# Kernel optimization log

Measured on AMD Instinct MI355X. Metric: run time of the kernel, lower is better.

The kernel has to match this reference:

```python
import jax, jax.numpy as jnp
import numpy as np

I_DIM, K_DIM, V_DIM, O_DIM = 64, 64, 32, 64
P, NH, NK = 7, 2, 4
B, H, W = 8, 256, 256


def get_unfold_params_v2(width, kernel_size, num_kernels):
    # exact replica of the torch helper's search
    if width <= kernel_size:
        return width, 1, 1, 1
    if width <= kernel_size + num_kernels:
        return kernel_size, 1, 1, width - kernel_size + 1

    def _sd(nk):
        d = 1
        while True:
            k = (kernel_size - 1) * d + 1
            if (width - k) % (nk - 1) == 0:
                return (width - k) // (nk - 1), d
            d += 1
            if d >= kernel_size:
                return None, d

    while True:
        s, d = _sd(num_kernels)
        if s and s < (kernel_size - 1) * d + 1:
            return kernel_size, s, d, num_kernels
        num_kernels += 1


def conv1x1(x, Wt, b):
    # x: [B,C,H,W], Wt: [O,C]
    return jnp.einsum('oc,bchw->bohw', Wt, x) + b[None, :, None, None]


def to_patches(x, nh, idx, p):
    # x: [B,C,H,W] -> [B, nh, nph*npw, C//nh, p*p] (unfold + rearrange)
    Bs, C, _, _ = x.shape
    hd = C // nh
    npw = idx.shape[0]
    pt = x[:, :, idx][:, :, :, :, idx]          # [B,C,nph,ph,npw,pw]
    pt = pt.reshape(Bs, nh, hd, npw, p, npw, p)
    pt = pt.transpose(0, 1, 3, 5, 2, 4, 6)       # B,nh,nph,npw,hd,ph,pw
    return pt.reshape(Bs, nh, npw * npw, hd, p * p)


def from_patches(o, nh, idx, p, Hh, Ww):
    # o: [B,nh,S,hd,p*p] -> fold (overlap scatter-add) -> [B, nh*hd, H, W]
    Bs, _, _, hd, _ = o.shape
    npw = idx.shape[0]
    o = o.reshape(Bs, nh, npw, npw, hd, p, p)
    o = o.transpose(0, 1, 4, 2, 5, 3, 6)         # B,nh,hd,nph,ph,npw,pw
    o = o.reshape(Bs, nh * hd, npw, p, npw, p)
    out = jnp.zeros((Bs, nh * hd, Hh, Ww), o.dtype)
    return out.at[:, :, idx[:, :, None, None], idx[None, None, :, :]].add(o)


def setup_inputs() -> dict:
    key = jax.random.key(0)
    ks = jax.random.split(key, 8)
    s = 0.05
    return {
        'x1': jax.random.normal(ks[0], (B, I_DIM, H, W), jnp.float32),
        'x2': jax.random.normal(ks[1], (B, I_DIM, H, W), jnp.float32),
        'Wk': jax.random.normal(ks[2], (2 * K_DIM, I_DIM), jnp.float32) * s,
        'bk': jax.random.normal(ks[3], (2 * K_DIM,), jnp.float32) * s,
        'Wv': jax.random.normal(ks[4], (2 * V_DIM, I_DIM), jnp.float32) * s,
        'bv': jax.random.normal(ks[5], (2 * V_DIM,), jnp.float32) * s,
        'Wp': jax.random.normal(ks[6], (O_DIM, 2 * V_DIM), jnp.float32) * s,
        'bp': jax.random.normal(ks[7], (O_DIM,), jnp.float32) * s,
    }


def reference(x1, x2, Wk, bk, Wv, bv, Wp, bp):
    _, _, Hh, Ww = x1.shape
    p, stride, dilation, nkrn = get_unfold_params_v2(Ww, P, NK)
    idx = np.arange(nkrn)[:, None] * stride + np.arange(p)[None, :] * dilation  # [npw,p]

    # grouped 1x1 convs (groups=2): split weights into per-stream halves
    k1 = conv1x1(x1, Wk[:K_DIM], bk[:K_DIM])
    k2 = conv1x1(x2, Wk[K_DIM:], bk[K_DIM:])
    v1 = conv1x1(x1, Wv[:V_DIM], bv[:V_DIM])
    v2 = conv1x1(x2, Wv[V_DIM:], bv[V_DIM:])

    k1p = to_patches(k1, NH, idx, p)  # [B,nh,S,hd_k,pp]
    k2p = to_patches(k2, NH, idx, p)
    v1p = to_patches(v1, NH, idx, p)  # [B,nh,S,hd_v,pp]
    v2p = to_patches(v2, NH, idx, p)

    scale = k1p.shape[-2] ** (-0.5)
    kk = jnp.einsum('bnsdx,bnsdy->bnsxy', k1p * scale, k2p)  # [B,nh,S,pp,pp]
    a1 = jax.nn.softmax(kk, axis=-2)
    o1 = jnp.einsum('bnsxy,bnsdx->bnsdy', a1, v1p)
    a2 = jax.nn.softmax(kk, axis=-1)
    o2 = jnp.einsum('bnsxy,bnsdy->bnsdx', a2, v2p)

    o1 = from_patches(o1, NH, idx, p, Hh, Ww)  # [B,V_DIM,H,W]
    o2 = from_patches(o2, NH, idx, p, Hh, Ww)
    o = jnp.concatenate([o1, o2], axis=1)      # [B,2*V_DIM,H,W]
    return conv1x1(o, Wp, bp)                  # [B,O_DIM,H,W]
```

## Files before the change

### kernel.cpp

```cpp
#include <hip/hip_runtime.h>

#define BB 8
#define HH 256
#define CIN 64
#define NPW 12
#define SPP 144
#define PP 49
#define PDIM 7
#define STRIDE 21
#define DIL 4
#define NS 84

typedef __attribute__((ext_vector_type(8))) short bf16x8;
typedef __attribute__((ext_vector_type(4))) float f32x4;

#define MFMA(a, b, c) __builtin_amdgcn_mfma_f32_16x16x32_bf16((a), (b), (c), 0, 0, 0)

static __device__ __forceinline__ unsigned short f2bf(float f) {
  union { float f; unsigned u; } v; v.f = f;
  unsigned r = (v.u + 0x7fffu + ((v.u >> 16) & 1u)) >> 16;
  return (unsigned short)r;
}
static __device__ __forceinline__ float bf2f(unsigned short h) {
  union { unsigned u; float f; } v; v.u = ((unsigned)h) << 16;
  return v.f;
}
static __device__ __forceinline__ unsigned pk2(float a, float b) {
  return (unsigned)f2bf(a) | ((unsigned)f2bf(b) << 16);
}

__global__ __launch_bounds__(256, 3) void k1_fused(
    const float* __restrict__ x1, const float* __restrict__ x2,
    const float* __restrict__ Wk, const float* __restrict__ bk,
    const float* __restrict__ Wv, const float* __restrict__ bv,
    const float* __restrict__ Wp, float* __restrict__ P)
{
  __shared__ __align__(16) short uA[9216];
  __shared__ __align__(16) short uB[8704];
  __shared__ __align__(16) short sV[4096];
  __shared__ float sStat[4][2][64];

  const int tid = threadIdx.x;
  const int lane = tid & 63;
  const int wid = tid >> 6;
  const int l16 = lane & 15;
  const int l4 = lane >> 4;
  const int blk = blockIdx.x;
  const int b  = blk / SPP;
  const int sp = blk % SPP;
  const int pi = sp / NPW, pj = sp % NPW;
  const int h0 = pi * STRIDE, w0 = pj * STRIDE;

  for (int i = tid; i < 2 * CIN * PP; i += 256) {
    int src = i / (CIN * PP);
    int r = i - src * (CIN * PP);
    int c = r / PP, t = r - c * PP;
    int ph = t / PDIM, pw = t - ph * PDIM;
    const float* xp = src ? x2 : x1;
    float v = xp[(((size_t)b * CIN + c) * HH + (h0 + ph * DIL)) * HH + (w0 + pw * DIL)];
    uA[(src * 64 + t) * 64 + ((((c >> 3) ^ (t & 7)) << 3) | (c & 7))] = (short)f2bf(v);
  }
  for (int i = tid; i < 2 * 15 * 64; i += 256) {
    int src = i / (15 * 64);
    int r = i - src * 15 * 64;
    int t = 49 + (r >> 6);
    int c = r & 63;
    uA[(src * 64 + t) * 64 + c] = 0;
  }
  __syncthreads();

  {
    #pragma unroll
    for (int mi = 0; mi < 3; mi++) {
      const int m = wid * 3 + mi;
      const int r0 = m * 16;
      const int src = (m < 4) ? 0 : (m < 8 ? 1 : (m < 10 ? 0 : 1));
      const int rl = r0 + l16;
      const float* wrow = (r0 < 128) ? (Wk + (size_t)rl * 64)
                                     : (Wv + (size_t)(rl - 128) * 64);
      bf16x8 ahi[2], alo[2];
      #pragma unroll
      for (int kt = 0; kt < 2; kt++) {
        const float* wp8 = wrow + kt * 32 + l4 * 8;
        float4 wa = *(const float4*)wp8;
        float4 wb = *(const float4*)(wp8 + 4);
        float wf[8] = {wa.x, wa.y, wa.z, wa.w, wb.x, wb.y, wb.z, wb.w};
        #pragma unroll
        for (int j = 0; j < 8; j++) {
          unsigned short h = f2bf(wf[j]);
          ahi[kt][j] = (short)h;
          alo[kt][j] = (short)f2bf(wf[j] - bf2f(h));
        }
      }
      float bias[4];
      #pragma unroll
      for (int i = 0; i < 4; i++) {
        int rd = r0 + l4 * 4 + i;
        bias[i] = (r0 < 128) ? bk[rd] : bv[rd - 128];
      }
      #pragma unroll
      for (int nt = 0; nt < 4; nt++) {
        const int t = nt * 16 + l16;
        f32x4 acc = {0.f, 0.f, 0.f, 0.f};
        #pragma unroll
        for (int kt = 0; kt < 2; kt++) {
          bf16x8 xb = *(const bf16x8*)
              &uA[(src * 64 + t) * 64 + ((((kt << 2) + l4) ^ (t & 7)) << 3)];
          acc = MFMA(alo[kt], xb, acc);
          acc = MFMA(ahi[kt], xb, acc);
        }
        if (r0 < 128) {
          unsigned* p = (unsigned*)&uB[t * 136 + r0 + l4 * 4];
          p[0] = pk2(acc[0] + bias[0], acc[1] + bias[1]);
          p[1] = pk2(acc[2] + bias[2], acc[3] + bias[3]);
        } else {
          #pragma unroll
          for (int i = 0; i < 4; i++) {
            int rv = r0 - 128 + l4 * 4 + i;
            sV[rv * 64 + ((((t >> 3) ^ (rv & 7)) << 3) | (t & 7))] =
                (short)f2bf(acc[i] + bias[i]);
          }
        }
      }
    }
  }
  __syncthreads();

  const float scale = 0.17677669529663687f;

  {
    const int n = wid >> 1;
    #pragma unroll
    for (int xi = 0; xi < 2; xi++) {
      const int x0 = ((wid & 1) * 2 + xi) * 16;
      bf16x8 a = *(const bf16x8*)&uB[(x0 + l16) * 136 + n * 32 + l4 * 8];
      #pragma unroll
      for (int yt = 0; yt < 4; yt++) {
        const int y = yt * 16 + l16;
        bf16x8 bb = *(const bf16x8*)&uB[y * 136 + 64 + n * 32 + l4 * 8];
        f32x4 acc = {0.f, 0.f, 0.f, 0.f};
        acc = MFMA(a, bb, acc);
        #pragma unroll
        for (int i = 0; i < 4; i++) {
          int x = x0 + l4 * 4 + i;
          uA[(n * 64 + x) * 72 + y] = (short)f2bf(acc[i] * scale);
        }
      }
    }
  }
  __syncthreads();

  if (tid < 196) {
    int n = tid / 98;
    int r = tid % 98;
    int isRow = r >= 49;
    int j = r - (isRow ? 49 : 0);
    float mx = -1e30f;
    for (int k = 0; k < 49; k++) {
      float v = bf2f((unsigned short)uA[(n * 64 + (isRow ? j : k)) * 72 + (isRow ? k : j)]);
      mx = fmaxf(mx, v);
    }
    float sm = 0.f;
    for (int k = 0; k < 49; k++) {
      float v = bf2f((unsigned short)uA[(n * 64 + (isRow ? j : k)) * 72 + (isRow ? k : j)]);
      sm += __expf(v - mx);
    }
    int kind = isRow ? 2 : 0;
    sStat[kind][n][j] = mx;
    sStat[kind + 1][n][j] = 1.0f / sm;
  }
  __syncthreads();

  {
    const int n = wid >> 1;
    const int side = wid & 1;
    const int rv = side * 32 + n * 16 + l16;
    bf16x8 av[2];
    #pragma unroll
    for (int kt = 0; kt < 2; kt++)
      av[kt] = *(const bf16x8*)&sV[rv * 64 + ((((kt << 2) + l4) ^ (rv & 7)) << 3)];
    if (side == 0) {
      #pragma unroll
      for (int tt = 0; tt < 4; tt++) {
        const int t = tt * 16 + l16;
        const float cm = sStat[0][n][t], cs = sStat[1][n][t];
        f32x4 acc = {0.f, 0.f, 0.f, 0.f};
        #pragma unroll
        for (int kt = 0; kt < 2; kt++) {
          bf16x8 bfrag;
          #pragma unroll
          for (int j = 0; j < 8; j++) {
            const int x = kt * 32 + l4 * 8 + j;
            float v = bf2f((unsigned short)uA[(n * 64 + x) * 72 + t]);
            float e = (x < PP) ? __expf(v - cm) : 0.f;
            bfrag[j] = (short)f2bf(e);
          }
          acc = MFMA(av[kt], bfrag, acc);
        }
        unsigned* p = (unsigned*)&uB[t * 72 + n * 16 + l4 * 4];
        p[0] = pk2(acc[0] * cs, acc[1] * cs);
        p[1] = pk2(acc[2] * cs, acc[3] * cs);
      }
    } else {
      #pragma unroll
      for (int xt = 0; xt < 4; xt++) {
        const int x = xt * 16 + l16;
        const float rm = sStat[2][n][x], rs = sStat[3][n][x];
        f32x4 acc = {0.f, 0.f, 0.f, 0.f};
        #pragma unroll
        for (int kt = 0; kt < 2; kt++) {
          bf16x8 braw = *(const bf16x8*)&uA[(n * 64 + x) * 72 + kt * 32 + l4 * 8];
          bf16x8 bfrag;
          #pragma unroll
          for (int j = 0; j < 8; j++) {
            const int y = kt * 32 + l4 * 8 + j;
            float v = bf2f((unsigned short)braw[j]);
            float e = (y < PP) ? __expf(v - rm) : 0.f;
            bfrag[j] = (short)f2bf(e);
          }
          acc = MFMA(av[kt], bfrag, acc);
        }
        unsigned* p = (unsigned*)&uB[x * 72 + 32 + n * 16 + l4 * 4];
        p[0] = pk2(acc[0] * rs, acc[1] * rs);
        p[1] = pk2(acc[2] * rs, acc[3] * rs);
      }
    }
  }
  __syncthreads();

  {
    const float* wrow = Wp + (size_t)(wid * 16 + l16) * 64;
    bf16x8 whi[2], wlo[2];
    #pragma unroll
    for (int kt = 0; kt < 2; kt++) {
      const float* wp8 = wrow + kt * 32 + l4 * 8;
      float4 wa = *(const float4*)wp8;
      float4 wb = *(const float4*)(wp8 + 4);
      float wf[8] = {wa.x, wa.y, wa.z, wa.w, wb.x, wb.y, wb.z, wb.w};
      #pragma unroll
      for (int j = 0; j < 8; j++) {
        unsigned short h = f2bf(wf[j]);
        whi[kt][j] = (short)h;
        wlo[kt][j] = (short)f2bf(wf[j] - bf2f(h));
      }
    }
    #pragma unroll
    for (int tt = 0; tt < 4; tt++) {
      const int t = tt * 16 + l16;
      f32x4 acc = {0.f, 0.f, 0.f, 0.f};
      #pragma unroll
      for (int kt = 0; kt < 2; kt++) {
        bf16x8 ob = *(const bf16x8*)&uB[t * 72 + kt * 32 + l4 * 8];
        acc = MFMA(wlo[kt], ob, acc);
        acc = MFMA(whi[kt], ob, acc);
      }
      if (t < PP) {
        const int ph = t / 7, pw = t - ph * 7;
        const size_t col = (size_t)(pi * 7 + ph) * NS + (pj * 7 + pw);
        #pragma unroll
        for (int i = 0; i < 4; i++) {
          const int oc = wid * 16 + l4 * 4 + i;
          P[((size_t)b * 64 + oc) * (NS * NS) + col] = acc[i];
        }
      }
    }
  }
}

__global__ __launch_bounds__(256) void k2_merge(
    const float* __restrict__ P, const float* __restrict__ bp,
    float* __restrict__ out)
{
  __shared__ float bps[64];
  __shared__ int wsmap[256];
  const int tid = threadIdx.x;
  const int b = blockIdx.x / HH, h = blockIdx.x % HH;
  if (tid < 64) bps[tid] = bp[tid];
  {
    int w = tid, wsv = -1;
    for (int pj = 0; pj < NPW; pj++) {
      int r = w - pj * STRIDE;
      if (r >= 0 && r <= (PDIM - 1) * DIL && (r % DIL) == 0) { wsv = pj * PDIM + r / DIL; break; }
    }
    wsmap[tid] = wsv;
  }
  int hs = -1;
  for (int pi = 0; pi < NPW; pi++) {
    int r = h - pi * STRIDE;
    if (r >= 0 && r <= (PDIM - 1) * DIL && (r % DIL) == 0) { hs = pi * PDIM + r / DIL; break; }
  }
  __syncthreads();

  const int wq = tid & 63;
  const int ocq = tid >> 6;
  float4* out4 = (float4*)out;

  if (hs < 0) {
    #pragma unroll 4
    for (int oc = ocq; oc < 64; oc += 4) {
      float bv = bps[oc];
      out4[(((size_t)b * 64 + oc) * HH + h) * 64 + wq] = make_float4(bv, bv, bv, bv);
    }
    return;
  }
  const int ws0 = wsmap[wq * 4 + 0], ws1 = wsmap[wq * 4 + 1];
  const int ws2 = wsmap[wq * 4 + 2], ws3 = wsmap[wq * 4 + 3];
  #pragma unroll 4
  for (int oc = ocq; oc < 64; oc += 4) {
    float bv = bps[oc];
    size_t rbase = (((size_t)b * 64 + oc) * NS + hs) * NS;
    float4 v = make_float4(bv, bv, bv, bv);
    if (ws0 >= 0) v.x += P[rbase + ws0];
    if (ws1 >= 0) v.y += P[rbase + ws1];
    if (ws2 >= 0) v.z += P[rbase + ws2];
    if (ws3 >= 0) v.w += P[rbase + ws3];
    out4[(((size_t)b * 64 + oc) * HH + h) * 64 + wq] = v;
  }
}

extern "C" void kernel_launch(void* const* d_in, const int* in_sizes, int n_in,
                              void* d_out, int out_size, void* d_ws, size_t ws_size,
                              hipStream_t stream) {
  const float* x1 = (const float*)d_in[0];
  const float* x2 = (const float*)d_in[1];
  const float* Wk = (const float*)d_in[2];
  const float* bk = (const float*)d_in[3];
  const float* Wv = (const float*)d_in[4];
  const float* bv = (const float*)d_in[5];
  const float* Wp = (const float*)d_in[6];
  const float* bp = (const float*)d_in[7];
  float* P = (float*)d_ws;
  float* out = (float*)d_out;

  k1_fused<<<dim3(BB * SPP), dim3(256), 0, stream>>>(x1, x2, Wk, bk, Wv, bv, Wp, P);
  k2_merge<<<dim3(BB * HH), dim3(256), 0, stream>>>(P, bp, out);
}
```

Baseline: 332.9 us.

## Merge LDS buffers into one swizzled arena and restructure patch gather

Folds the four separate shared-memory arrays into one 40KB arena with aliased regions and XOR-swizzled layouts everywhere, which cuts LDS per block so four blocks can fit per CU (launch bounds raised from 3 to 4). The input gather now has each thread fetch 25 strided values for one channel in registers before writing them, replacing the div/mod-heavy loop. Padding rows are zeroed with word stores. The risks are more register pressure from the 25-value buffer under the tighter occupancy bound, and correctness depending on the aliasing lifetimes of the reused regions.

```diff
diff --git a/kernel.cpp b/kernel.cpp
--- a/kernel.cpp
+++ b/kernel.cpp
@@ -28,17 +28,17 @@
 static __device__ __forceinline__ unsigned pk2(float a, float b) {
   return (unsigned)f2bf(a) | ((unsigned)f2bf(b) << 16);
 }
-
-__global__ __launch_bounds__(256, 3) void k1_fused(
+static __device__ __forceinline__ int swz(int col, int row) {
+  return ((((col >> 3) ^ (row & 7)) & 7) << 3) | (col & 7);
+}
+
+__global__ __launch_bounds__(256, 4) void k1_fused(
     const float* __restrict__ x1, const float* __restrict__ x2,
     const float* __restrict__ Wk, const float* __restrict__ bk,
     const float* __restrict__ Wv, const float* __restrict__ bv,
     const float* __restrict__ Wp, float* __restrict__ P)
 {
-  __shared__ __align__(16) short uA[9216];
-  __shared__ __align__(16) short uB[8704];
-  __shared__ __align__(16) short sV[4096];
-  __shared__ float sStat[4][2][64];
+  __shared__ __align__(16) short lds[20480];
 
   const int tid = threadIdx.x;
   const int lane = tid & 63;
@@ -51,21 +51,31 @@
   const int pi = sp / NPW, pj = sp % NPW;
   const int h0 = pi * STRIDE, w0 = pj * STRIDE;
 
-  for (int i = tid; i < 2 * CIN * PP; i += 256) {
-    int src = i / (CIN * PP);
-    int r = i - src * (CIN * PP);
-    int c = r / PP, t = r - c * PP;
-    int ph = t / PDIM, pw = t - ph * PDIM;
+  {
+    const int c = tid & 63;
+    const int g = tid >> 6;
+    const int src = g >> 1;
+    const int half = g & 1;
+    const int t0 = half * 24;
     const float* xp = src ? x2 : x1;
-    float v = xp[(((size_t)b * CIN + c) * HH + (h0 + ph * DIL)) * HH + (w0 + pw * DIL)];
-    uA[(src * 64 + t) * 64 + ((((c >> 3) ^ (t & 7)) << 3) | (c & 7))] = (short)f2bf(v);
-  }
-  for (int i = tid; i < 2 * 15 * 64; i += 256) {
-    int src = i / (15 * 64);
-    int r = i - src * 15 * 64;
-    int t = 49 + (r >> 6);
-    int c = r & 63;
-    uA[(src * 64 + t) * 64 + c] = 0;
+    int pw = half ? 3 : 0;
+    const int ph = half ? 3 : 0;
+    const float* p = xp + (((size_t)(b * CIN + c)) * HH + (h0 + ph * DIL)) * HH
+                     + (w0 + pw * DIL);
+    float vals[25];
+    #pragma unroll
+    for (int q = 0; q < 25; ++q) {
+      vals[q] = *p;
+      ++pw; p += DIL;
+      if (pw == PDIM) { pw = 0; p += DIL * HH - PDIM * DIL; }
+    }
+    #pragma unroll
+    for (int q = 0; q < 25; ++q) {
+      const int t = t0 + q;
+      lds[(src * 64 + t) * 64 + swz(c, t)] = (short)f2bf(vals[q]);
+    }
+    unsigned* z = (unsigned*)lds;
+    for (int i = tid; i < 480; i += 256) { z[1568 + i] = 0u; z[3616 + i] = 0u; }
   }
   __syncthreads();
 
@@ -105,20 +115,22 @@
         #pragma unroll
         for (int kt = 0; kt < 2; kt++) {
           bf16x8 xb = *(const bf16x8*)
-              &uA[(src * 64 + t) * 64 + ((((kt << 2) + l4) ^ (t & 7)) << 3)];
+              &lds[(src * 64 + t) * 64 + ((((kt << 2) + l4) ^ (t & 7)) << 3)];
           acc = MFMA(alo[kt], xb, acc);
           acc = MFMA(ahi[kt], xb, acc);
         }
         if (r0 < 128) {
-          unsigned* p = (unsigned*)&uB[t * 136 + r0 + l4 * 4];
+          const int rcol = r0 + l4 * 4;
+          const int base = (rcol < 64) ? 8192 : 12288;
+          const int col = rcol & 63;
+          unsigned* p = (unsigned*)&lds[base + t * 64 + swz(col, t)];
           p[0] = pk2(acc[0] + bias[0], acc[1] + bias[1]);
           p[1] = pk2(acc[2] + bias[2], acc[3] + bias[3]);
         } else {
           #pragma unroll
           for (int i = 0; i < 4; i++) {
             int rv = r0 - 128 + l4 * 4 + i;
-            sV[rv * 64 + ((((t >> 3) ^ (rv & 7)) << 3) | (t & 7))] =
-                (short)f2bf(acc[i] + bias[i]);
+            lds[16384 + rv * 64 + swz(t, rv)] = (short)f2bf(acc[i] + bias[i]);
           }
         }
       }
@@ -133,57 +145,68 @@
     #pragma unroll
     for (int xi = 0; xi < 2; xi++) {
       const int x0 = ((wid & 1) * 2 + xi) * 16;
-      bf16x8 a = *(const bf16x8*)&uB[(x0 + l16) * 136 + n * 32 + l4 * 8];
+      const int tA = x0 + l16;
+      bf16x8 a = *(const bf16x8*)
+          &lds[8192 + tA * 64 + ((((n << 2) + l4) ^ (tA & 7)) << 3)];
       #pragma unroll
       for (int yt = 0; yt < 4; yt++) {
         const int y = yt * 16 + l16;
-        bf16x8 bb = *(const bf16x8*)&uB[y * 136 + 64 + n * 32 + l4 * 8];
+        bf16x8 bb = *(const bf16x8*)
+            &lds[12288 + y * 64 + ((((n << 2) + l4) ^ (y & 7)) << 3)];
         f32x4 acc = {0.f, 0.f, 0.f, 0.f};
         acc = MFMA(a, bb, acc);
         #pragma unroll
         for (int i = 0; i < 4; i++) {
           int x = x0 + l4 * 4 + i;
-          uA[(n * 64 + x) * 72 + y] = (short)f2bf(acc[i] * scale);
-        }
-      }
-    }
-  }
-  __syncthreads();
-
-  if (tid < 196) {
-    int n = tid / 98;
-    int r = tid % 98;
-    int isRow = r >= 49;
-    int j = r - (isRow ? 49 : 0);
-    float mx = -1e30f;
-    for (int k = 0; k < 49; k++) {
-      float v = bf2f((unsigned short)uA[(n * 64 + (isRow ? j : k)) * 72 + (isRow ? k : j)]);
-      mx = fmaxf(mx, v);
-    }
-    float sm = 0.f;
-    for (int k = 0; k < 49; k++) {
-      float v = bf2f((unsigned short)uA[(n * 64 + (isRow ? j : k)) * 72 + (isRow ? k : j)]);
-      sm += __expf(v - mx);
-    }
-    int kind = isRow ? 2 : 0;
-    sStat[kind][n][j] = mx;
-    sStat[kind + 1][n][j] = 1.0f / sm;
-  }
-  __syncthreads();
-
-  {
+          lds[(n * 64 + x) * 64 + swz(y, x)] = (short)f2bf(acc[i] * scale);
+        }
+      }
+    }
+  }
+  __syncthreads();
+
+  {
+    float* sStat = (float*)&lds[12288];
+    if (tid < 196) {
+      int n = tid / 98;
+      int r = tid % 98;
+      int isRow = r >= 49;
+      int j = r - (isRow ? 49 : 0);
+      float mx = -1e30f;
+      for (int k = 0; k < 49; k++) {
+        int xr = isRow ? j : k, yc = isRow ? k : j;
+        float v = bf2f((unsigned short)lds[(n * 64 + xr) * 64 + swz(yc, xr)]);
+        mx = fmaxf(mx, v);
+      }
+      float sm = 0.f;
+      for (int k = 0; k < 49; k++) {
+        int xr = isRow ? j : k, yc = isRow ? k : j;
+        float v = bf2f((unsigned short)lds[(n * 64 + xr) * 64 + swz(yc, xr)]);
+        sm += __expf(v - mx);
+      }
+      int kind = isRow ? 2 : 0;
+      sStat[(kind * 2 + n) * 64 + j] = mx;
+      sStat[((kind + 1) * 2 + n) * 64 + j] = 1.0f / sm;
+    }
+  }
+  __syncthreads();
+
+  {
+    const float* sStat = (const float*)&lds[12288];
     const int n = wid >> 1;
     const int side = wid & 1;
     const int rv = side * 32 + n * 16 + l16;
     bf16x8 av[2];
     #pragma unroll
     for (int kt = 0; kt < 2; kt++)
-      av[kt] = *(const bf16x8*)&sV[rv * 64 + ((((kt << 2) + l4) ^ (rv & 7)) << 3)];
+      av[kt] = *(const bf16x8*)
+          &lds[16384 + rv * 64 + ((((kt << 2) + l4) ^ (rv & 7)) << 3)];
     if (side == 0) {
       #pragma unroll
       for (int tt = 0; tt < 4; tt++) {
         const int t = tt * 16 + l16;
-        const float cm = sStat[0][n][t], cs = sStat[1][n][t];
+        const float cm = sStat[(0 * 2 + n) * 64 + t];
+        const float cs = sStat[(1 * 2 + n) * 64 + t];
         f32x4 acc = {0.f, 0.f, 0.f, 0.f};
         #pragma unroll
         for (int kt = 0; kt < 2; kt++) {
@@ -191,13 +214,14 @@
           #pragma unroll
           for (int j = 0; j < 8; j++) {
             const int x = kt * 32 + l4 * 8 + j;
-            float v = bf2f((unsigned short)uA[(n * 64 + x) * 72 + t]);
+            float v = bf2f((unsigned short)lds[(n * 64 + x) * 64 + swz(t, x)]);
             float e = (x < PP) ? __expf(v - cm) : 0.f;
             bfrag[j] = (short)f2bf(e);
           }
           acc = MFMA(av[kt], bfrag, acc);
         }
-        unsigned* p = (unsigned*)&uB[t * 72 + n * 16 + l4 * 4];
+        const int col = n * 16 + l4 * 4;
+        unsigned* p = (unsigned*)&lds[8192 + t * 64 + swz(col, t)];
         p[0] = pk2(acc[0] * cs, acc[1] * cs);
         p[1] = pk2(acc[2] * cs, acc[3] * cs);
       }
@@ -205,11 +229,13 @@
       #pragma unroll
       for (int xt = 0; xt < 4; xt++) {
         const int x = xt * 16 + l16;
-        const float rm = sStat[2][n][x], rs = sStat[3][n][x];
+        const float rm = sStat[(2 * 2 + n) * 64 + x];
+        const float rs = sStat[(3 * 2 + n) * 64 + x];
         f32x4 acc = {0.f, 0.f, 0.f, 0.f};
         #pragma unroll
         for (int kt = 0; kt < 2; kt++) {
-          bf16x8 braw = *(const bf16x8*)&uA[(n * 64 + x) * 72 + kt * 32 + l4 * 8];
+          bf16x8 braw = *(const bf16x8*)
+              &lds[(n * 64 + x) * 64 + ((((kt << 2) + l4) ^ (x & 7)) << 3)];
           bf16x8 bfrag;
           #pragma unroll
           for (int j = 0; j < 8; j++) {
@@ -220,7 +246,8 @@
           }
           acc = MFMA(av[kt], bfrag, acc);
         }
-        unsigned* p = (unsigned*)&uB[x * 72 + 32 + n * 16 + l4 * 4];
+        const int col = 32 + n * 16 + l4 * 4;
+        unsigned* p = (unsigned*)&lds[8192 + x * 64 + swz(col, x)];
         p[0] = pk2(acc[0] * rs, acc[1] * rs);
         p[1] = pk2(acc[2] * rs, acc[3] * rs);
       }
@@ -250,7 +277,8 @@
       f32x4 acc = {0.f, 0.f, 0.f, 0.f};
       #pragma unroll
       for (int kt = 0; kt < 2; kt++) {
-        bf16x8 ob = *(const bf16x8*)&uB[t * 72 + kt * 32 + l4 * 8];
+        bf16x8 ob = *(const bf16x8*)
+            &lds[8192 + t * 64 + ((((kt << 2) + l4) ^ (t & 7)) << 3)];
         acc = MFMA(wlo[kt], ob, acc);
         acc = MFMA(whi[kt], ob, acc);
       }
```

Measured after the change: 335.1 us. No clear change (+0.6%).
